# Kernel optimization log

Measured on AMD Instinct MI355X. Metric: run time of the kernel, lower is better.

The kernel has to match this reference:

```python
import math
import jax, jax.numpy as jnp
import numpy as np

B, NV, C = 8, 512, 256
H, R = 6, 32
PAIR_H = 16
RBF_K = 8


def setup_inputs() -> dict:
    key = jax.random.key(0)
    ks = jax.random.split(key, 12)
    s = lambda fan_in: 1.0 / math.sqrt(fan_in)
    inp = {
        'feats': jax.random.normal(ks[0], (B, 2 * NV + 1, C), jnp.float32),
        'xy': jax.random.uniform(ks[1], (B, NV, 2), jnp.float32),
        'Wq': jax.random.normal(ks[2], (C, H * R), jnp.float32) * s(C),
        'Wk': jax.random.normal(ks[3], (C, H * R), jnp.float32) * s(C),
        'Wpi': jax.random.normal(ks[4], (C, PAIR_H), jnp.float32) * s(C),
        'bpi': jnp.zeros((PAIR_H,), jnp.float32),
        'Wpj': jax.random.normal(ks[5], (C, PAIR_H), jnp.float32) * s(C),
        'bpj': jnp.zeros((PAIR_H,), jnp.float32),
        'gW1': jax.random.normal(ks[6], (2 + RBF_K + 2, 32), jnp.float32) * s(12),
        'gb1': jnp.zeros((32,), jnp.float32),
        'gW2': jax.random.normal(ks[7], (32, 1), jnp.float32) * s(32),
        'gb2': jnp.zeros((1,), jnp.float32),
        'aW1': jax.random.normal(ks[8], (6, 16), jnp.float32) * s(6),
        'ab1': jnp.zeros((16,), jnp.float32),
        'aW2': jax.random.normal(ks[9], (16, 1), jnp.float32) * s(16),
        'ab2': jnp.zeros((1,), jnp.float32),
        'dW': jax.random.normal(ks[10], (C, 1), jnp.float32) * s(C),
        'db': jnp.zeros((1,), jnp.float32),
        'alpha_pair': jnp.float32(0.5),
        'alpha_geom': jnp.float32(0.6),
        'alpha_angle': jnp.float32(0.6),
        'logit_scale': jnp.float32(1.0),
    }
    return inp


def _pos_scale(p, lo=0.0, hi=1.5):
    return lo + (hi - lo) * jax.nn.sigmoid(p)


def _logit_scale_fn(p, lo=0.5, hi=3.0):
    return lo + (hi - lo) * jax.nn.sigmoid(p)


def reference(feats, xy, Wq, Wk, Wpi, bpi, Wpj, bpj, gW1, gb1, gW2, gb2,
              aW1, ab1, aW2, ab2, dW, db,
              alpha_pair, alpha_geom, alpha_angle, logit_scale):
    # fold vertices: drop BOS, average (y, x) token pairs -> [B, N, C]
    x = feats[:, 1:]
    Bb, L, Cc = x.shape
    x = x.reshape(Bb, L // 2, 2, Cc).mean(axis=2)
    N = x.shape[1]

    # multi-head low-rank bilinear core, summed over heads
    Q = (x @ Wq).reshape(Bb, N, H, R)
    K = (x @ Wk).reshape(Bb, N, H, R)
    S = jnp.einsum('bnhr,bmhr->bnm', Q, K) / math.sqrt(R)

    # separable pair nonlinearity (outer product of tiny ReLU features)
    a_i = jax.nn.relu(x @ Wpi + bpi)
    b_j = jax.nn.relu(x @ Wpj + bpj)
    S = S + _pos_scale(alpha_pair) * jnp.einsum('bnd,bmd->bnm', a_i, b_j)

    # geometry / angle biases
    yv, xv = xy[..., 0], xy[..., 1]
    dy = yv[:, :, None] - yv[:, None, :]          # [B,N,N]
    dx = xv[:, :, None] - xv[:, None, :]
    theta = jnp.arctan2(dy, dx)
    pad_i = (jnp.abs(yv) < 1e-9) & (jnp.abs(xv) < 1e-9)
    pad_pair = pad_i[:, :, None] | pad_i[:, None, :]
    c1, s1 = jnp.cos(theta), jnp.sin(theta)

    # distance RBF + cos/sin bias
    rbf_mu = jnp.linspace(0.0, math.sqrt(2.0), RBF_K).astype(jnp.float32)
    spacing = rbf_mu[1] - rbf_mu[0]
    rbf_gamma = 1.0 / (2.0 * spacing ** 2 + 1e-8)
    r = jnp.sqrt(dy * dy + dx * dx + 1e-8)
    phi = jnp.exp(-rbf_gamma * (r[..., None] - rbf_mu) ** 2)  # [B,N,N,K]
    geom_feat = jnp.concatenate(
        [dy[..., None], dx[..., None], phi, c1[..., None], s1[..., None]], axis=-1)
    G = (jax.nn.relu(geom_feat @ gW1 + gb1) @ gW2 + gb2)[..., 0]
    G = jnp.where(pad_pair, 0.0, G)
    S = S + _pos_scale(alpha_geom) * G

    # angle harmonics (theta, 2theta, 4theta)
    c2, s2 = jnp.cos(2.0 * theta), jnp.sin(2.0 * theta)
    c4, s4 = jnp.cos(4.0 * theta), jnp.sin(4.0 * theta)
    ang_feat = jnp.stack([c1, s1, c2, s2, c4, s4], axis=-1)  # [B,N,N,6]
    Hb = (jax.nn.relu(ang_feat @ aW1 + ab1) @ aW2 + ab2)[..., 0]
    Hb = jnp.where(pad_pair, 0.0, Hb)
    S = S + _pos_scale(alpha_angle) * Hb

    # diagonal bias and bounded global scale
    d = (x @ dW + db)[..., 0]                     # [B,N]
    idx = jnp.arange(N)
    S = S.at[:, idx, idx].add(d)
    S = S * _logit_scale_fn(logit_scale)
    return S
```

## Files before the change

### kernel.cpp

```cpp
#include <hip/hip_runtime.h>
#include <math.h>


#define UK 224

typedef __attribute__((ext_vector_type(8)))  short short8;
typedef __attribute__((ext_vector_type(16))) float f32x16;
typedef __attribute__((ext_vector_type(4)))  int   int4v;

__device__ __forceinline__ float sigmoidf_(float x){ return 1.0f/(1.0f + __expf(-x)); }
__device__ __forceinline__ unsigned f2bf(float x){
    unsigned u = __builtin_bit_cast(unsigned, x);
    return (u + 0x7fffu + ((u>>16)&1u)) >> 16;
}
__device__ __forceinline__ unsigned pk2(float lo, float hi){
    unsigned r;
    asm("v_cvt_pk_bf16_f32 %0, %1, %2" : "=v"(r) : "v"(lo), "v"(hi));
    return r;
}
__device__ __forceinline__ f32x16 zero16(){
    f32x16 z;
    #pragma unroll
    for (int i = 0; i < 16; i++) z[i] = 0.f;
    return z;
}

__global__ __launch_bounds__(256) void k_prep(const float* __restrict__ feats,
        const float* __restrict__ Wq, const float* __restrict__ Wk,
        const float* __restrict__ Wpi, const float* __restrict__ bpi,
        const float* __restrict__ Wpj, const float* __restrict__ bpj,
        const float* __restrict__ dW, const float* __restrict__ db,
        const float* __restrict__ a_pair,
        unsigned short* __restrict__ xb, unsigned short* __restrict__ WT,
        float* __restrict__ bcat){
    int blk = blockIdx.x, tid = threadIdx.x;
    if (blk < 4096){
        int b = blk >> 9, n = blk & 511;
        size_t base = ((size_t)(b*1025 + 1 + 2*n))*256 + tid;
        float v = 0.5f*(feats[base] + feats[base+256]);
        xb[(size_t)blk*256 + tid] = (unsigned short)f2bf(v);
    } else {
        int col = blk - 4096;
        int c   = tid;
        const float invSqrtR = 0.17677669529663687f;
        float sp = 1.5f*sigmoidf_(a_pair[0]);
        float v;
        if      (col < 192)  v = Wq[c*192 + col]*invSqrtR;
        else if (col < 208)  v = sp*Wpi[c*16 + (col-192)];
        else if (col < 400)  v = Wk[c*192 + (col-208)];
        else if (col < 416)  v = Wpj[c*16 + (col-400)];
        else if (col == 416) v = dW[c];
        else v = 0.f;
        WT[col*256 + c] = (unsigned short)f2bf(v);
        if (tid == 0){
            float bv = 0.f;
            if      (col >= 192 && col < 208) bv = sp*bpi[col-192];
            else if (col >= 400 && col < 416) bv = bpj[col-400];
            else if (col == 416)              bv = db[0];
            bcat[col] = bv;
        }
    }
}

__global__ __launch_bounds__(256) void k_uv(const unsigned short* __restrict__ xb,
        const unsigned short* __restrict__ WT, const float* __restrict__ bcat,
        unsigned short* __restrict__ Ub, unsigned short* __restrict__ Vb,
        float* __restrict__ dv){
    int tid = threadIdx.x;
    int lane = tid & 63, l31 = lane & 31, hf = lane >> 5;
    int w = tid >> 6, wr = w >> 1, wc = w & 1;
    int c0 = blockIdx.x*64, r0 = blockIdx.y*64;
    const unsigned short* ap = xb + (size_t)(r0 + wr*32 + l31)*256 + 8*hf;
    const unsigned short* bp = WT + (size_t)(c0 + wc*32 + l31)*256 + 8*hf;
    f32x16 acc = zero16();
    #pragma unroll 4
    for (int k0 = 0; k0 < 256; k0 += 16){
        short8 a  = *(const short8*)(ap + k0);
        short8 bb = *(const short8*)(bp + k0);
        acc = __builtin_amdgcn_mfma_f32_32x32x16_bf16(a, bb, acc, 0, 0, 0);
    }
    int col = c0 + wc*32 + l31;
    int rb  = r0 + wr*32 + 4*hf;
    float bc = bcat[col];
    #pragma unroll
    for (int r = 0; r < 16; r++){
        int row = rb + (r&3) + 8*(r>>2);
        float v = acc[r] + bc;
        size_t ui = (size_t)row*UK;
        if (col < 208){
            if (col >= 192) v = fmaxf(v, 0.f);
            Ub[ui + col] = (unsigned short)f2bf(v);
        } else if (col < 224){
            Vb[ui + col-208] = (unsigned short)f2bf(v);
            Ub[ui + col] = 0;
        } else if (col < 416){
            if (col >= 400) v = fmaxf(v, 0.f);
            Vb[ui + col-208] = (unsigned short)f2bf(v);
        } else if (col == 416){
            dv[row] = v;
            Vb[ui + 208] = 0;
        } else if (col < 432){
            Vb[ui + col-208] = 0;
        }
    }
}

__global__ __launch_bounds__(256, 3) void k_gp(const unsigned short* __restrict__ Ub,
        const unsigned short* __restrict__ Vb, const float* __restrict__ xy,
        const float* __restrict__ gW1, const float* __restrict__ gb1,
        const float* __restrict__ gW2, const float* __restrict__ gb2,
        const float* __restrict__ aW1, const float* __restrict__ ab1,
        const float* __restrict__ aW2, const float* __restrict__ ab2,
        const float* __restrict__ dv,
        const float* __restrict__ a_geom, const float* __restrict__ a_ang,
        const float* __restrict__ lsc,
        float* __restrict__ S){
    __shared__ float acc_lds[64][64];
    int tid = threadIdx.x;
    int lane = tid & 63, l31 = lane & 31, hf = lane >> 5;
    int w = tid >> 6, wr = w >> 1, wc = w & 1;
    int b = blockIdx.z;
    int m0 = blockIdx.x*64, n0 = blockIdx.y*64;

    {
        const unsigned short* ap = Ub + (size_t)(b*512 + n0 + wr*32 + l31)*UK + 8*hf;
        const unsigned short* bp = Vb + (size_t)(b*512 + m0 + wc*32 + l31)*UK + 8*hf;
        f32x16 acc = zero16();
        #pragma unroll 2
        for (int k0 = 0; k0 < UK; k0 += 16){
            short8 a  = *(const short8*)(ap + k0);
            short8 bb = *(const short8*)(bp + k0);
            acc = __builtin_amdgcn_mfma_f32_32x32x16_bf16(a, bb, acc, 0, 0, 0);
        }
        int colL = wc*32 + l31;
        int rbL  = wr*32 + 4*hf;
        #pragma unroll
        for (int r = 0; r < 16; r++)
            acc_lds[rbL + (r&3) + 8*(r>>2)][colL] = acc[r];
    }
    __syncthreads();

    float sg = 1.5f*sigmoidf_(a_geom[0]);
    float sa = 1.5f*sigmoidf_(a_ang[0]);
    float ls = 0.5f + 2.5f*sigmoidf_(lsc[0]);

    short8 wg, wa;
    #pragma unroll
    for (int j = 0; j < 8; j++){
        int f = hf*8 + j;
        float vg = (f < 12) ? gW1[f*32 + l31] : 0.f;
        float va = (f >= 10 && l31 < 16) ? aW1[(f-10)*16 + l31] : 0.f;
        wg[j] = (short)f2bf(vg);
        wa[j] = (short)f2bf(va);
    }
    float nbg[16], g2g[16], nba[16], g2a[16];
    float bsum = 0.f;
    #pragma unroll
    for (int r = 0; r < 16; r++){
        int h = (r&3) + 8*(r>>2) + 4*hf;
        float bg  = gb1[h];
        float wg2 = sg*gW2[h];
        nbg[r] = -bg; g2g[r] = wg2; bsum += bg*wg2;
        if (h < 16){
            float ba  = ab1[h];
            float wa2 = sa*aW2[h];
            nba[r] = -ba; g2a[r] = wa2; bsum += ba*wa2;
        } else { nba[r] = 0.f; g2a[r] = 0.f; }
    }
    bsum += __shfl_xor(bsum, 32);
    float cb = sg*gb2[0] + sa*ab2[0] + bsum;

    const float GAMMA = 12.2499985f;
    const float TWOGD = 4.9497469f;
    const float* xyb = xy + (size_t)b*1024;

    int m_w = m0 + lane;
    float2 pmv = *(const float2*)(xyb + 2*m_w);
    float ym = pmv.x, xm = pmv.y;
    bool padm = (fabsf(ym) < 1e-9f) && (fabsf(xm) < 1e-9f);

    for (int i = 0; i < 16; i++){
        int nrow = (w << 4) + i;
        int nn = n0 + nrow;
        float yn = xyb[2*nn], xn = xyb[2*nn+1];
        bool padn = (fabsf(yn) < 1e-9f) && (fabsf(xn) < 1e-9f);
        float msk = (padn || padm) ? 0.f : 1.f;

        float dy = yn - ym, dx = xn - xm;
        float r2 = dy*dy + dx*dx;
        float re = sqrtf(r2 + 1e-8f);
        float c1, s1;
        if (r2 > 0.f){ float inv = rsqrtf(r2); c1 = dx*inv; s1 = dy*inv; }
        else { c1 = 1.f; s1 = 0.f; }
        float c2 = c1*c1 - s1*s1, s2 = 2.f*c1*s1;
        float c4 = c2*c2 - s2*s2, s4 = 2.f*c2*s2;
        float e0 = __expf(-GAMMA*(r2 + 1e-8f));
        float E  = __expf(TWOGD*re);
        float u  = e0;
        float p0 = u;
        u *= E; float p1 = 0.60653066f*u;
        u *= E; float p2 = 0.13533528f*u;
        u *= E; float p3 = 0.011108997f*u;
        u *= E; float p4 = 3.3546263e-4f*u;
        u *= E; float p5 = 3.7266532e-6f*u;
        u *= E; float p6 = 1.5229979e-8f*u;
        u *= E; float p7 = 2.2897348e-11f*u;
        unsigned pk0 = pk2(dy, dx), pk1 = pk2(p0, p1), pk2_ = pk2(p2, p3), pk3 = pk2(p4, p5);
        unsigned pk4 = pk2(p6, p7), pk5 = pk2(c1, s1), pk6 = pk2(c2, s2), pk7 = pk2(c4, s4);

        int s0 = __shfl_xor((int)(hf ? pk0 : pk4), 32);
        int s1i= __shfl_xor((int)(hf ? pk1 : pk5), 32);
        int s2i= __shfl_xor((int)(hf ? pk2_: pk6), 32);
        int s3i= __shfl_xor((int)(hf ? pk3 : pk7), 32);

        int fA0 = hf ? s0 : (int)pk0, fA1 = hf ? s1i : (int)pk1;
        int fA2 = hf ? s2i : (int)pk2_, fA3 = hf ? s3i : (int)pk3;
        int fB0 = hf ? (int)pk4 : s0,  fB1 = hf ? (int)pk5 : s1i;
        int fB2 = hf ? (int)pk6 : s2i, fB3 = hf ? (int)pk7 : s3i;
        int4v ivA = {fA0, fA1, fA2, fA3};
        int4v ivB = {fB0, fB1, fB2, fB3};
        short8 bfA = __builtin_bit_cast(short8, ivA);
        short8 bfB = __builtin_bit_cast(short8, ivB);

        f32x16 z = zero16();
        f32x16 dgA = __builtin_amdgcn_mfma_f32_32x32x16_bf16(wg, bfA, z, 0, 0, 0);
        f32x16 dgB = __builtin_amdgcn_mfma_f32_32x32x16_bf16(wg, bfB, z, 0, 0, 0);
        f32x16 daA = __builtin_amdgcn_mfma_f32_32x32x16_bf16(wa, bfA, z, 0, 0, 0);
        f32x16 daB = __builtin_amdgcn_mfma_f32_32x32x16_bf16(wa, bfB, z, 0, 0, 0);

        float a0=0.f,a1=0.f,a2=0.f,a3=0.f,b0=0.f,b1=0.f,b2=0.f,b3=0.f;
        #pragma unroll
        for (int r = 0; r < 8; r++){
            a0 += fmaxf(dgA[r],   nbg[r])   * g2g[r];
            a1 += fmaxf(dgA[r+8], nbg[r+8]) * g2g[r+8];
            b0 += fmaxf(dgB[r],   nbg[r])   * g2g[r];
            b1 += fmaxf(dgB[r+8], nbg[r+8]) * g2g[r+8];
            a2 += fmaxf(daA[r],   nba[r])   * g2a[r];
            a3 += fmaxf(daA[r+8], nba[r+8]) * g2a[r+8];
            b2 += fmaxf(daB[r],   nba[r])   * g2a[r];
            b3 += fmaxf(daB[r+8], nba[r+8]) * g2a[r+8];
        }
        float accA = (a0 + a1) + (a2 + a3);
        float accB = (b0 + b1) + (b2 + b3);
        accA += __shfl_xor(accA, 32);
        accB += __shfl_xor(accB, 32);

        float res = (lane < 32) ? accA : accB;
        acc_lds[nrow][lane] += msk*(res + cb);
    }
    __syncthreads();

    {
        int m  = m0 + wc*32 + l31;
        int rbL = wr*32 + 4*hf;
        float* Sp = S + ((size_t)b*512)*512 + m;
        #pragma unroll
        for (int r = 0; r < 16; r++){
            int nloc = rbL + (r&3) + 8*(r>>2);
            int n = n0 + nloc;
            float v = acc_lds[nloc][wc*32 + l31];
            if (m == n) v += dv[b*512 + n];
            Sp[(size_t)n*512] = v * ls;
        }
    }
}

extern "C" void kernel_launch(void* const* d_in, const int* in_sizes, int n_in,
                              void* d_out, int out_size, void* d_ws, size_t ws_size,
                              hipStream_t stream){
    const float* feats = (const float*)d_in[0];
    const float* xy    = (const float*)d_in[1];
    const float* Wq    = (const float*)d_in[2];
    const float* Wk    = (const float*)d_in[3];
    const float* Wpi   = (const float*)d_in[4];
    const float* bpi   = (const float*)d_in[5];
    const float* Wpj   = (const float*)d_in[6];
    const float* bpj   = (const float*)d_in[7];
    const float* gW1   = (const float*)d_in[8];
    const float* gb1   = (const float*)d_in[9];
    const float* gW2   = (const float*)d_in[10];
    const float* gb2   = (const float*)d_in[11];
    const float* aW1   = (const float*)d_in[12];
    const float* ab1   = (const float*)d_in[13];
    const float* aW2   = (const float*)d_in[14];
    const float* ab2   = (const float*)d_in[15];
    const float* dW    = (const float*)d_in[16];
    const float* db    = (const float*)d_in[17];
    const float* a_pair= (const float*)d_in[18];
    const float* a_geom= (const float*)d_in[19];
    const float* a_ang = (const float*)d_in[20];
    const float* lsc   = (const float*)d_in[21];

    float* S = (float*)d_out;
    char* wsb = (char*)d_ws;
    unsigned short* xb = (unsigned short*)wsb;
    unsigned short* WT = (unsigned short*)(wsb + 2097152);
    unsigned short* Ub = (unsigned short*)(wsb + 2326528);
    unsigned short* Vb = (unsigned short*)(wsb + 4161536);
    float* bcat = (float*)(wsb + 5996544);
    float* dv   = (float*)(wsb + 5998336);

    k_prep <<<4544, 256, 0, stream>>>(feats, Wq, Wk, Wpi, bpi, Wpj, bpj, dW, db, a_pair,
                                      xb, WT, bcat);
    k_uv   <<<dim3(7,64), 256, 0, stream>>>(xb, WT, bcat, Ub, Vb, dv);
    k_gp   <<<dim3(8,8,8), 256, 0, stream>>>(Ub, Vb, xy, gW1, gb1, gW2, gb2,
                                             aW1, ab1, aW2, ab2, dv,
                                             a_geom, a_ang, lsc, S);
}
```

Before: 52.07 us.

## Halve k_gp row tile and split MFMA K-dimension across wave pairs

The k_gp tile shrinks from 64x64 to 32x64 output rows, doubling the grid to 1024 blocks. The 224-wide K reduction is split in half between the two wave rows, and their partial sums are combined through two LDS buffers. The final store is rewritten to use row-contiguous, coalesced writes. The aim is more blocks for occupancy and less per-block geometry work, at the cost of recomputing per-block setup and reloading V tiles twice as often.

```diff
diff --git a/kernel.cpp b/kernel.cpp
--- a/kernel.cpp
+++ b/kernel.cpp
@@ -115,28 +115,27 @@
         const float* __restrict__ a_geom, const float* __restrict__ a_ang,
         const float* __restrict__ lsc,
         float* __restrict__ S){
-    __shared__ float acc_lds[64][64];
+    __shared__ float acc_lds[2][32][64];
     int tid = threadIdx.x;
     int lane = tid & 63, l31 = lane & 31, hf = lane >> 5;
     int w = tid >> 6, wr = w >> 1, wc = w & 1;
     int b = blockIdx.z;
-    int m0 = blockIdx.x*64, n0 = blockIdx.y*64;
+    int m0 = blockIdx.x*64, n0 = blockIdx.y*32;
 
     {
-        const unsigned short* ap = Ub + (size_t)(b*512 + n0 + wr*32 + l31)*UK + 8*hf;
-        const unsigned short* bp = Vb + (size_t)(b*512 + m0 + wc*32 + l31)*UK + 8*hf;
+        const unsigned short* ap = Ub + (size_t)(b*512 + n0 + l31)*UK + wr*112 + 8*hf;
+        const unsigned short* bp = Vb + (size_t)(b*512 + m0 + wc*32 + l31)*UK + wr*112 + 8*hf;
         f32x16 acc = zero16();
-        #pragma unroll 2
-        for (int k0 = 0; k0 < UK; k0 += 16){
-            short8 a  = *(const short8*)(ap + k0);
-            short8 bb = *(const short8*)(bp + k0);
+        #pragma unroll
+        for (int t = 0; t < 7; t++){
+            short8 a  = *(const short8*)(ap + t*16);
+            short8 bb = *(const short8*)(bp + t*16);
             acc = __builtin_amdgcn_mfma_f32_32x32x16_bf16(a, bb, acc, 0, 0, 0);
         }
         int colL = wc*32 + l31;
-        int rbL  = wr*32 + 4*hf;
         #pragma unroll
         for (int r = 0; r < 16; r++)
-            acc_lds[rbL + (r&3) + 8*(r>>2)][colL] = acc[r];
+            acc_lds[wr][(r&3) + 8*(r>>2) + 4*hf][colL] = acc[r];
     }
     __syncthreads();
 
@@ -179,8 +178,8 @@
     float ym = pmv.x, xm = pmv.y;
     bool padm = (fabsf(ym) < 1e-9f) && (fabsf(xm) < 1e-9f);
 
-    for (int i = 0; i < 16; i++){
-        int nrow = (w << 4) + i;
+    for (int i = 0; i < 8; i++){
+        int nrow = (w << 3) + i;
         int nn = n0 + nrow;
         float yn = xyb[2*nn], xn = xyb[2*nn+1];
         bool padn = (fabsf(yn) < 1e-9f) && (fabsf(xn) < 1e-9f);
@@ -246,22 +245,22 @@
         accB += __shfl_xor(accB, 32);
 
         float res = (lane < 32) ? accA : accB;
-        acc_lds[nrow][lane] += msk*(res + cb);
+        acc_lds[0][nrow][lane] += msk*(res + cb);
     }
     __syncthreads();
 
     {
-        int m  = m0 + wc*32 + l31;
-        int rbL = wr*32 + 4*hf;
-        float* Sp = S + ((size_t)b*512)*512 + m;
+        float dvb = 0.f;
         #pragma unroll
-        for (int r = 0; r < 16; r++){
-            int nloc = rbL + (r&3) + 8*(r>>2);
-            int n = n0 + nloc;
-            float v = acc_lds[nloc][wc*32 + l31];
+        for (int j = 0; j < 8; j++){
+            int flat = tid + j*256;
+            int row = flat >> 6, col = flat & 63;
+            float v = acc_lds[0][row][col] + acc_lds[1][row][col];
+            int n = n0 + row, m = m0 + col;
             if (m == n) v += dv[b*512 + n];
-            Sp[(size_t)n*512] = v * ls;
-        }
+            S[((size_t)b*512 + n)*512 + m] = v * ls;
+        }
+        (void)dvb;
     }
 }
 
@@ -303,7 +302,7 @@
     k_prep <<<4544, 256, 0, stream>>>(feats, Wq, Wk, Wpi, bpi, Wpj, bpj, dW, db, a_pair,
                                       xb, WT, bcat);
     k_uv   <<<dim3(7,64), 256, 0, stream>>>(xb, WT, bcat, Ub, Vb, dv);
-    k_gp   <<<dim3(8,8,8), 256, 0, stream>>>(Ub, Vb, xy, gW1, gb1, gW2, gb2,
-                                             aW1, ab1, aW2, ab2, dv,
-                                             a_geom, a_ang, lsc, S);
-}
+    k_gp   <<<dim3(8,16,8), 256, 0, stream>>>(Ub, Vb, xy, gW1, gb1, gW2, gb2,
+                                              aW1, ab1, aW2, ab2, dv,
+                                              a_geom, a_ang, lsc, S);
+}
```

New measurement: 50.75 us. 2.6% less time.
